# Performance work log

Measured on AMD Instinct MI355X. Metric: run time of the kernel, lower is better.

Reference implementation:

```python
import jax, jax.numpy as jnp
import numpy as np

CONTEXT = 2048
D_MODEL = 1024
HEAD = 64


def setup_inputs() -> dict:
    key = jax.random.key(0)
    kx, kk, kq, kv = jax.random.split(key, 4)
    s = 1.0 / np.sqrt(D_MODEL)  # ~ torch Linear init scale
    return {
        "x": jax.random.normal(kx, (8, CONTEXT, D_MODEL), dtype=jnp.float32),
        "Wk": jax.random.uniform(kk, (D_MODEL, HEAD), dtype=jnp.float32, minval=-s, maxval=s),
        "Wq": jax.random.uniform(kq, (D_MODEL, HEAD), dtype=jnp.float32, minval=-s, maxval=s),
        "Wv": jax.random.uniform(kv, (D_MODEL, HEAD), dtype=jnp.float32, minval=-s, maxval=s),
    }


def reference(x, Wk, Wq, Wv):
    b, t, c = x.shape
    k = jnp.einsum("btc,ch->bth", x, Wk)
    q = jnp.einsum("btc,ch->bth", x, Wq)
    v = jnp.einsum("btc,ch->bth", x, Wv)
    # NOTE: original scales by c**-0.5 (embedding dim), not head_size**-0.5
    scores = jnp.einsum("bqh,bkh->bqk", q, k) * (c ** -0.5)
    causal = jnp.tril(jnp.ones((t, t), dtype=bool))
    scores = jnp.where(causal, scores, jnp.float32(-jnp.inf))
    weights = jax.nn.softmax(scores, axis=-1)
    return jnp.einsum("bqk,bkh->bqh", weights, v)
```

## Files before the change

kernel.cpp:

```cpp
#include <hip/hip_runtime.h>
#include <hip/hip_bf16.h>

#define CTX 2048
#define DM  1024
#define HD  64
#define BATCH 8
#define NSLOT 144

typedef __attribute__((ext_vector_type(8))) short bf16x8;
typedef __attribute__((ext_vector_type(4))) float f32x4;

__device__ inline unsigned short f2bf(float f) {
    unsigned int u = __float_as_uint(f);
    unsigned int r = (u + 0x7fffu + ((u >> 16) & 1u)) >> 16;
    return (unsigned short)r;
}

__device__ inline bf16x8 pack8(const float4& f0, const float4& f1) {
    union { bf16x8 v; __hip_bfloat162 h[4]; } u;
    u.h[0] = __float22bfloat162_rn(make_float2(f0.x, f0.y));
    u.h[1] = __float22bfloat162_rn(make_float2(f0.z, f0.w));
    u.h[2] = __float22bfloat162_rn(make_float2(f1.x, f1.y));
    u.h[3] = __float22bfloat162_rn(make_float2(f1.z, f1.w));
    return u.v;
}

__device__ __forceinline__ int chunk_prefix(int qi) {
    int q4 = qi >> 2, r = qi & 3;
    return qi + 2 * q4 * (q4 - 1) + q4 * r;
}

__global__ __launch_bounds__(256) void wtrans(
    const float* __restrict__ Wq, const float* __restrict__ Wk,
    const float* __restrict__ Wv, unsigned short* __restrict__ wt)
{
    __shared__ __align__(16) unsigned short tile[64][72];
    const int m  = blockIdx.y;
    const int k0 = blockIdx.x * 64;
    const float* W = (m == 0) ? Wq : (m == 1) ? Wk : Wv;
    const int tid = threadIdx.x;
    const int c   = tid & 63, kk = tid >> 6;
    #pragma unroll
    for (int i = 0; i < 16; i++) {
        int kl = kk + i * 4;
        tile[c][kl] = f2bf(W[(size_t)(k0 + kl) * HD + c]);
    }
    __syncthreads();
    const int c2 = tid >> 2, seg = tid & 3;
    bf16x8 a = *reinterpret_cast<const bf16x8*>(&tile[c2][seg * 16]);
    bf16x8 b = *reinterpret_cast<const bf16x8*>(&tile[c2][seg * 16 + 8]);
    unsigned short* dst = wt + (size_t)(m * 64 + c2) * DM + k0 + seg * 16;
    *reinterpret_cast<bf16x8*>(dst)     = a;
    *reinterpret_cast<bf16x8*>(dst + 8) = b;
}

__global__ __launch_bounds__(512) void qkv_gemm(
    const float* __restrict__ x, const unsigned short* __restrict__ wt,
    unsigned short* __restrict__ q, unsigned short* __restrict__ k,
    unsigned short* __restrict__ vt)
{
    __shared__ __align__(16) unsigned short wsT[2][192 * 64];
    __shared__ __align__(16) unsigned short xsB[2][32 * 64];

    const int tid  = threadIdx.x, lane = tid & 63, w = tid >> 6;
    const int wr   = w >> 2, wc = w & 3;
    const int m0   = (int)blockIdx.x * 32;
    const int lcol = lane & 15, g = lane >> 4;

    const int wc_c   = tid >> 3;
    const int wc_par = tid & 7;
    const int xrow   = tid >> 3;
    const int xpar   = tid & 7;

    f32x4 acc[3];
    #pragma unroll
    for (int cf = 0; cf < 3; cf++) acc[cf] = (f32x4)0.f;

    bf16x8 rwA[3], rwB[3];
    float4 rxA0, rxA1, rxB0, rxB1;

    auto ldA = [&](int k0) {
        #pragma unroll
        for (int i = 0; i < 3; i++)
            rwA[i] = *reinterpret_cast<const bf16x8*>(wt + (size_t)(wc_c + i * 64) * DM + k0 + wc_par * 8);
        if (tid < 256) {
            const float* src = x + (size_t)(m0 + xrow) * DM + k0 + xpar * 8;
            rxA0 = *reinterpret_cast<const float4*>(src);
            rxA1 = *reinterpret_cast<const float4*>(src + 4);
        }
    };
    auto ldB = [&](int k0) {
        #pragma unroll
        for (int i = 0; i < 3; i++)
            rwB[i] = *reinterpret_cast<const bf16x8*>(wt + (size_t)(wc_c + i * 64) * DM + k0 + wc_par * 8);
        if (tid < 256) {
            const float* src = x + (size_t)(m0 + xrow) * DM + k0 + xpar * 8;
            rxB0 = *reinterpret_cast<const float4*>(src);
            rxB1 = *reinterpret_cast<const float4*>(src + 4);
        }
    };
    auto stA = [&](int buf) {
        char* wb = reinterpret_cast<char*>(wsT[buf]);
        char* xb = reinterpret_cast<char*>(xsB[buf]);
        #pragma unroll
        for (int i = 0; i < 3; i++) {
            int c = wc_c + i * 64;
            *reinterpret_cast<bf16x8*>(wb + ((c * 128 + wc_par * 16) ^ ((c & 7) << 4))) = rwA[i];
        }
        if (tid < 256)
            *reinterpret_cast<bf16x8*>(xb + ((xrow * 128 + xpar * 16) ^ ((xrow & 7) << 4))) = pack8(rxA0, rxA1);
    };
    auto stB = [&](int buf) {
        char* wb = reinterpret_cast<char*>(wsT[buf]);
        char* xb = reinterpret_cast<char*>(xsB[buf]);
        #pragma unroll
        for (int i = 0; i < 3; i++) {
            int c = wc_c + i * 64;
            *reinterpret_cast<bf16x8*>(wb + ((c * 128 + wc_par * 16) ^ ((c & 7) << 4))) = rwB[i];
        }
        if (tid < 256)
            *reinterpret_cast<bf16x8*>(xb + ((xrow * 128 + xpar * 16) ^ ((xrow & 7) << 4))) = pack8(rxB0, rxB1);
    };
    auto compute = [&](int buf) {
        char* wb = reinterpret_cast<char*>(wsT[buf]);
        char* xb = reinterpret_cast<char*>(xsB[buf]);
        #pragma unroll
        for (int kc = 0; kc < 2; kc++) {
            const int arow = wr * 16 + lcol;
            bf16x8 a = *reinterpret_cast<const bf16x8*>(
                xb + ((arow * 128 + kc * 64 + g * 16) ^ ((arow & 7) << 4)));
            #pragma unroll
            for (int cf = 0; cf < 3; cf++) {
                const int c = wc * 48 + cf * 16 + lcol;
                bf16x8 b = *reinterpret_cast<const bf16x8*>(
                    wb + ((c * 128 + kc * 64 + g * 16) ^ ((c & 7) << 4)));
                acc[cf] = __builtin_amdgcn_mfma_f32_16x16x32_bf16(a, b, acc[cf], 0, 0, 0);
            }
        }
    };

    ldA(0); ldB(64);
    stA(0);
    __syncthreads();

    #pragma unroll 1
    for (int t = 0; t < 16; t += 2) {
        if (t + 2 < 16) ldA((t + 2) * 64);
        compute(0);
        stB(1);
        __syncthreads();
        if (t + 3 < 16) ldB((t + 3) * 64);
        compute(1);
        if (t + 2 < 16) stA(0);
        __syncthreads();
    }

    const float QSCALE = 0.03125f * 1.4426950408889634f;
    #pragma unroll
    for (int cf = 0; cf < 3; cf++)
        #pragma unroll
        for (int r = 0; r < 4; r++) {
            int row = m0 + wr * 16 + g * 4 + r;
            int col = wc * 48 + cf * 16 + lcol;
            int bb = row >> 11, tt = row & (CTX - 1);
            if (col < 64)       q[(size_t)row * HD + col] = f2bf(acc[cf][r] * QSCALE);
            else if (col < 128) k[(size_t)row * HD + (col - 64)] = f2bf(acc[cf][r]);
            else                vt[(size_t)bb * HD * CTX + (size_t)(col - 128) * CTX + tt] = f2bf(acc[cf][r]);
        }
}

__global__ __launch_bounds__(256) void attn_fa(
    const unsigned short* __restrict__ qg, const unsigned short* __restrict__ kg,
    const unsigned short* __restrict__ vtg, unsigned short* __restrict__ po,
    float* __restrict__ ml)
{
    __shared__ __align__(16) unsigned short ks[64 * 64];
    __shared__ __align__(16) unsigned short vs[64 * 64];
    __shared__ __align__(16) float pf[4][16][68];

    const int tid  = threadIdx.x, lane = tid & 63, w = tid >> 6;
    const int bid  = blockIdx.x;
    const int b    = blockIdx.y;
    int qi = 31;
    while (chunk_prefix(qi) > bid) qi--;
    const int c  = bid - chunk_prefix(qi);
    const int t0 = c * 4, t1 = min(t0 + 3, qi);
    const int rb = qi * 64 + w * 16;
    const int lcol = lane & 15, g = lane >> 4, lrow = g << 2;
    const size_t base  = (size_t)b * CTX * HD;
    const size_t vbase = (size_t)b * HD * CTX;
    char* ksb = reinterpret_cast<char*>(ks);
    char* vsb = reinterpret_cast<char*>(vs);

    bf16x8 qa[2];
    #pragma unroll
    for (int kc = 0; kc < 2; kc++)
        qa[kc] = *reinterpret_cast<const bf16x8*>(
            qg + base + (size_t)(rb + lcol) * HD + kc * 32 + 8 * g);

    f32x4 o[4];
    #pragma unroll
    for (int dc = 0; dc < 4; dc++) o[dc] = (f32x4)0.f;
    float lsum[4] = {0.f, 0.f, 0.f, 0.f};

    const int r0 = tid >> 3, p0 = tid & 7, r1 = 32 + r0;
    bf16x8 kreg0, kreg1, vreg0, vreg1;

    auto ld = [&](int t) {
        const int j0 = t * 64;
        kreg0 = *reinterpret_cast<const bf16x8*>(kg + base + (size_t)(j0 + r0) * HD + p0 * 8);
        kreg1 = *reinterpret_cast<const bf16x8*>(kg + base + (size_t)(j0 + r1) * HD + p0 * 8);
        vreg0 = *reinterpret_cast<const bf16x8*>(vtg + vbase + (size_t)r0 * CTX + j0 + p0 * 8);
        vreg1 = *reinterpret_cast<const bf16x8*>(vtg + vbase + (size_t)r1 * CTX + j0 + p0 * 8);
    };
    auto st = [&]() {
        *reinterpret_cast<bf16x8*>(ksb + ((r0 * 128 + p0 * 16) ^ ((r0 & 7) << 4))) = kreg0;
        *reinterpret_cast<bf16x8*>(ksb + ((r1 * 128 + p0 * 16) ^ ((r1 & 7) << 4))) = kreg1;
        *reinterpret_cast<bf16x8*>(vsb + ((r0 * 128 + p0 * 16) ^ ((r0 & 7) << 4))) = vreg0;
        *reinterpret_cast<bf16x8*>(vsb + ((r1 * 128 + p0 * 16) ^ ((r1 & 7) << 4))) = vreg1;
    };

    ld(t0);
    for (int t = t0; t <= t1; t++) {
        __syncthreads();
        st();
        __syncthreads();
        if (t < t1) ld(t + 1);
        const int j0 = t * 64;

        f32x4 s[4];
        #pragma unroll
        for (int ch = 0; ch < 4; ch++) {
            s[ch] = (f32x4)0.f;
            #pragma unroll
            for (int kc = 0; kc < 2; kc++) {
                const int krow = ch * 16 + lcol;
                bf16x8 kf = *reinterpret_cast<const bf16x8*>(
                    ksb + ((krow * 128 + kc * 64 + g * 16) ^ ((krow & 7) << 4)));
                s[ch] = __builtin_amdgcn_mfma_f32_16x16x32_bf16(qa[kc], kf, s[ch], 0, 0, 0);
            }
        }

        if (t == qi) {
            #pragma unroll
            for (int ch = 0; ch < 4; ch++)
                #pragma unroll
                for (int r = 0; r < 4; r++)
                    if (j0 + ch * 16 + lcol > rb + lrow + r) s[ch][r] = -1e30f;
        }

        #pragma unroll
        for (int ch = 0; ch < 4; ch++)
            #pragma unroll
            for (int r = 0; r < 4; r++) {
                float p = exp2f(s[ch][r]);
                lsum[r] += p;
                pf[w][lrow + r][ch * 16 + lcol] = p;
            }

        bf16x8 pa[2];
        #pragma unroll
        for (int kc = 0; kc < 2; kc++) {
            const float* prow = &pf[w][lcol][0];
            float4 f0 = *reinterpret_cast<const float4*>(prow + kc * 32 + 8 * g);
            float4 f1 = *reinterpret_cast<const float4*>(prow + kc * 32 + 8 * g + 4);
            pa[kc] = pack8(f0, f1);
        }

        #pragma unroll
        for (int dc = 0; dc < 4; dc++)
            #pragma unroll
            for (int kc = 0; kc < 2; kc++) {
                const int vrow = dc * 16 + lcol;
                bf16x8 vf = *reinterpret_cast<const bf16x8*>(
                    vsb + ((vrow * 128 + kc * 64 + g * 16) ^ ((vrow & 7) << 4)));
                o[dc] = __builtin_amdgcn_mfma_f32_16x16x32_bf16(pa[kc], vf, o[dc], 0, 0, 0);
            }
    }

    const size_t sl = (size_t)b * NSLOT + bid;
    #pragma unroll
    for (int dc = 0; dc < 4; dc++)
        #pragma unroll
        for (int r = 0; r < 4; r++)
            po[sl * 4096 + (size_t)(w * 16 + lrow + r) * 64 + dc * 16 + lcol] = f2bf(o[dc][r]);
    #pragma unroll
    for (int r = 0; r < 4; r++) {
        float x = lsum[r];
        x += __shfl_xor(x, 1);
        x += __shfl_xor(x, 2);
        x += __shfl_xor(x, 4);
        x += __shfl_xor(x, 8);
        lsum[r] = x;
    }
    if (lcol == 0) {
        #pragma unroll
        for (int r = 0; r < 4; r++)
            ml[sl * 64 + w * 16 + lrow + r] = lsum[r];
    }
}

__global__ __launch_bounds__(256) void attn_merge(
    const unsigned short* __restrict__ po, const float* __restrict__ ml,
    float* __restrict__ out)
{
    const int qi = blockIdx.x, b = blockIdx.y;
    const int nch = (qi >> 2) + 1;
    const int s0  = chunk_prefix(qi);
    const int f8  = threadIdx.x & 7;
    const int r0  = threadIdx.x >> 3;
    const size_t obase = (size_t)b * CTX * HD;

    #pragma unroll
    for (int half = 0; half < 2; half++) {
        const int row = half * 32 + r0;
        float L = 0.f;
        float acc[8];
        #pragma unroll
        for (int j = 0; j < 8; j++) acc[j] = 0.f;
        for (int cc = 0; cc < nch; cc++) {
            size_t sl = (size_t)b * NSLOT + s0 + cc;
            L += ml[sl * 64 + row];
            bf16x8 v8 = *reinterpret_cast<const bf16x8*>(po + sl * 4096 + (size_t)row * 64 + f8 * 8);
            #pragma unroll
            for (int j = 0; j < 8; j++)
                acc[j] += __uint_as_float(((unsigned)(unsigned short)v8[j]) << 16);
        }
        const float inv = 1.f / L;
        float4 o0 = make_float4(acc[0] * inv, acc[1] * inv, acc[2] * inv, acc[3] * inv);
        float4 o1 = make_float4(acc[4] * inv, acc[5] * inv, acc[6] * inv, acc[7] * inv);
        float* dst = out + obase + (size_t)(qi * 64 + row) * HD + f8 * 8;
        *reinterpret_cast<float4*>(dst)     = o0;
        *reinterpret_cast<float4*>(dst + 4) = o1;
    }
}

extern "C" void kernel_launch(void* const* d_in, const int* in_sizes, int n_in,
                              void* d_out, int out_size, void* d_ws, size_t ws_size,
                              hipStream_t stream) {
    const float* x  = (const float*)d_in[0];
    const float* Wk = (const float*)d_in[1];
    const float* Wq = (const float*)d_in[2];
    const float* Wv = (const float*)d_in[3];
    float* outp = (float*)d_out;

    const size_t n = (size_t)BATCH * CTX * HD;
    unsigned short* qb  = (unsigned short*)d_ws;
    unsigned short* kb  = qb + n;
    unsigned short* vtb = kb + n;
    unsigned short* wtb = vtb + n;
    unsigned short* pob = wtb + 192 * 1024;
    float*          mlb = (float*)(pob + (size_t)BATCH * NSLOT * 4096);

    wtrans<<<dim3(16, 3), dim3(256), 0, stream>>>(Wq, Wk, Wv, wtb);
    qkv_gemm<<<dim3(16384 / 32), dim3(512), 0, stream>>>(x, wtb, qb, kb, vtb);
    attn_fa<<<dim3(NSLOT, BATCH), dim3(256), 0, stream>>>(qb, kb, vtb, pob, mlb);
    attn_merge<<<dim3(32, BATCH), dim3(256), 0, stream>>>(pob, mlb, outp);
}
```

Baseline: 53.90 us.

## Read QKV weights directly from global, swizzle P buffer, vectorize partial-output stores

```diff
diff --git a/kernel.cpp b/kernel.cpp
--- a/kernel.cpp
+++ b/kernel.cpp
@@ -23,6 +23,15 @@
     u.h[2] = __float22bfloat162_rn(make_float2(f1.x, f1.y));
     u.h[3] = __float22bfloat162_rn(make_float2(f1.z, f1.w));
     return u.v;
+}
+
+__device__ inline uint2 pack4(const float4& f) {
+    __hip_bfloat162 h0 = __float22bfloat162_rn(make_float2(f.x, f.y));
+    __hip_bfloat162 h1 = __float22bfloat162_rn(make_float2(f.z, f.w));
+    uint2 r;
+    __builtin_memcpy(&r.x, &h0, 4);
+    __builtin_memcpy(&r.y, &h1, 4);
+    return r;
 }
 
 __device__ __forceinline__ int chunk_prefix(int qi) {
@@ -59,99 +68,58 @@
     unsigned short* __restrict__ q, unsigned short* __restrict__ k,
     unsigned short* __restrict__ vt)
 {
-    __shared__ __align__(16) unsigned short wsT[2][192 * 64];
-    __shared__ __align__(16) unsigned short xsB[2][32 * 64];
+    __shared__ __align__(16) unsigned short xs[2][32 * 64];
 
     const int tid  = threadIdx.x, lane = tid & 63, w = tid >> 6;
     const int wr   = w >> 2, wc = w & 3;
     const int m0   = (int)blockIdx.x * 32;
     const int lcol = lane & 15, g = lane >> 4;
 
-    const int wc_c   = tid >> 3;
-    const int wc_par = tid & 7;
-    const int xrow   = tid >> 3;
-    const int xpar   = tid & 7;
+    const int xrow = tid >> 4, xseg = tid & 15;
+    const float* xsrc = x + (size_t)(m0 + xrow) * DM + xseg * 4;
+    const int xoff = (xrow * 128 + xseg * 8) ^ ((xrow & 7) << 4);
+
+    const unsigned short* wbase = wt + (size_t)(wc * 48 + lcol) * DM + g * 8;
 
     f32x4 acc[3];
     #pragma unroll
     for (int cf = 0; cf < 3; cf++) acc[cf] = (f32x4)0.f;
 
-    bf16x8 rwA[3], rwB[3];
-    float4 rxA0, rxA1, rxB0, rxB1;
-
-    auto ldA = [&](int k0) {
-        #pragma unroll
-        for (int i = 0; i < 3; i++)
-            rwA[i] = *reinterpret_cast<const bf16x8*>(wt + (size_t)(wc_c + i * 64) * DM + k0 + wc_par * 8);
-        if (tid < 256) {
-            const float* src = x + (size_t)(m0 + xrow) * DM + k0 + xpar * 8;
-            rxA0 = *reinterpret_cast<const float4*>(src);
-            rxA1 = *reinterpret_cast<const float4*>(src + 4);
-        }
+    float4 ra, rb;
+    auto ld = [&](int k0) { return *reinterpret_cast<const float4*>(xsrc + k0); };
+    auto st = [&](const float4& v, int buf) {
+        *reinterpret_cast<uint2*>(reinterpret_cast<char*>(xs[buf]) + xoff) = pack4(v);
     };
-    auto ldB = [&](int k0) {
-        #pragma unroll
-        for (int i = 0; i < 3; i++)
-            rwB[i] = *reinterpret_cast<const bf16x8*>(wt + (size_t)(wc_c + i * 64) * DM + k0 + wc_par * 8);
-        if (tid < 256) {
-            const float* src = x + (size_t)(m0 + xrow) * DM + k0 + xpar * 8;
-            rxB0 = *reinterpret_cast<const float4*>(src);
-            rxB1 = *reinterpret_cast<const float4*>(src + 4);
-        }
-    };
-    auto stA = [&](int buf) {
-        char* wb = reinterpret_cast<char*>(wsT[buf]);
-        char* xb = reinterpret_cast<char*>(xsB[buf]);
-        #pragma unroll
-        for (int i = 0; i < 3; i++) {
-            int c = wc_c + i * 64;
-            *reinterpret_cast<bf16x8*>(wb + ((c * 128 + wc_par * 16) ^ ((c & 7) << 4))) = rwA[i];
-        }
-        if (tid < 256)
-            *reinterpret_cast<bf16x8*>(xb + ((xrow * 128 + xpar * 16) ^ ((xrow & 7) << 4))) = pack8(rxA0, rxA1);
-    };
-    auto stB = [&](int buf) {
-        char* wb = reinterpret_cast<char*>(wsT[buf]);
-        char* xb = reinterpret_cast<char*>(xsB[buf]);
-        #pragma unroll
-        for (int i = 0; i < 3; i++) {
-            int c = wc_c + i * 64;
-            *reinterpret_cast<bf16x8*>(wb + ((c * 128 + wc_par * 16) ^ ((c & 7) << 4))) = rwB[i];
-        }
-        if (tid < 256)
-            *reinterpret_cast<bf16x8*>(xb + ((xrow * 128 + xpar * 16) ^ ((xrow & 7) << 4))) = pack8(rxB0, rxB1);
-    };
-    auto compute = [&](int buf) {
-        char* wb = reinterpret_cast<char*>(wsT[buf]);
-        char* xb = reinterpret_cast<char*>(xsB[buf]);
+    auto compute = [&](int buf, int k0) {
+        char* xb = reinterpret_cast<char*>(xs[buf]);
+        const int arow = wr * 16 + lcol;
         #pragma unroll
         for (int kc = 0; kc < 2; kc++) {
-            const int arow = wr * 16 + lcol;
             bf16x8 a = *reinterpret_cast<const bf16x8*>(
                 xb + ((arow * 128 + kc * 64 + g * 16) ^ ((arow & 7) << 4)));
             #pragma unroll
             for (int cf = 0; cf < 3; cf++) {
-                const int c = wc * 48 + cf * 16 + lcol;
                 bf16x8 b = *reinterpret_cast<const bf16x8*>(
-                    wb + ((c * 128 + kc * 64 + g * 16) ^ ((c & 7) << 4)));
+                    wbase + (size_t)cf * 16 * DM + k0 + kc * 32);
                 acc[cf] = __builtin_amdgcn_mfma_f32_16x16x32_bf16(a, b, acc[cf], 0, 0, 0);
             }
         }
     };
 
-    ldA(0); ldB(64);
-    stA(0);
+    ra = ld(0);
+    rb = ld(64);
+    st(ra, 0);
     __syncthreads();
 
     #pragma unroll 1
     for (int t = 0; t < 16; t += 2) {
-        if (t + 2 < 16) ldA((t + 2) * 64);
-        compute(0);
-        stB(1);
+        if (t + 2 < 16) ra = ld((t + 2) * 64);
+        compute(0, t * 64);
+        st(rb, 1);
         __syncthreads();
-        if (t + 3 < 16) ldB((t + 3) * 64);
-        compute(1);
-        if (t + 2 < 16) stA(0);
+        if (t + 3 < 16) rb = ld((t + 3) * 64);
+        compute(1, (t + 1) * 64);
+        if (t + 2 < 16) st(ra, 0);
         __syncthreads();
     }
 
@@ -176,7 +144,7 @@
 {
     __shared__ __align__(16) unsigned short ks[64 * 64];
     __shared__ __align__(16) unsigned short vs[64 * 64];
-    __shared__ __align__(16) float pf[4][16][68];
+    __shared__ __align__(16) float pf[4][16 * 64];
 
     const int tid  = threadIdx.x, lane = tid & 63, w = tid >> 6;
     const int bid  = blockIdx.x;
@@ -191,6 +159,7 @@
     const size_t vbase = (size_t)b * HD * CTX;
     char* ksb = reinterpret_cast<char*>(ks);
     char* vsb = reinterpret_cast<char*>(vs);
+    char* pb  = reinterpret_cast<char*>(pf[w]);
 
     bf16x8 qa[2];
     #pragma unroll
@@ -255,15 +224,19 @@
             for (int r = 0; r < 4; r++) {
                 float p = exp2f(s[ch][r]);
                 lsum[r] += p;
-                pf[w][lrow + r][ch * 16 + lcol] = p;
+                const int row = lrow + r;
+                *reinterpret_cast<float*>(
+                    pb + ((row * 256 + (ch * 16 + lcol) * 4) ^ ((row & 7) << 4))) = p;
             }
 
         bf16x8 pa[2];
+        const int rswz = (lcol & 7) << 4;
         #pragma unroll
         for (int kc = 0; kc < 2; kc++) {
-            const float* prow = &pf[w][lcol][0];
-            float4 f0 = *reinterpret_cast<const float4*>(prow + kc * 32 + 8 * g);
-            float4 f1 = *reinterpret_cast<const float4*>(prow + kc * 32 + 8 * g + 4);
+            float4 f0 = *reinterpret_cast<const float4*>(
+                pb + ((lcol * 256 + kc * 128 + g * 32) ^ rswz));
+            float4 f1 = *reinterpret_cast<const float4*>(
+                pb + ((lcol * 256 + kc * 128 + g * 32 + 16) ^ rswz));
             pa[kc] = pack8(f0, f1);
         }
 
@@ -282,8 +255,22 @@
     #pragma unroll
     for (int dc = 0; dc < 4; dc++)
         #pragma unroll
-        for (int r = 0; r < 4; r++)
-            po[sl * 4096 + (size_t)(w * 16 + lrow + r) * 64 + dc * 16 + lcol] = f2bf(o[dc][r]);
+        for (int r = 0; r < 4; r++) {
+            const int row = lrow + r;
+            *reinterpret_cast<float*>(
+                pb + ((row * 256 + (dc * 16 + lcol) * 4) ^ ((row & 7) << 4))) = o[dc][r];
+        }
+    {
+        const int orow = lcol;
+        const int rswz = (orow & 7) << 4;
+        float4 a0 = *reinterpret_cast<const float4*>(pb + ((orow * 256 + g * 64)      ^ rswz));
+        float4 a1 = *reinterpret_cast<const float4*>(pb + ((orow * 256 + g * 64 + 16) ^ rswz));
+        float4 a2 = *reinterpret_cast<const float4*>(pb + ((orow * 256 + g * 64 + 32) ^ rswz));
+        float4 a3 = *reinterpret_cast<const float4*>(pb + ((orow * 256 + g * 64 + 48) ^ rswz));
+        unsigned short* dst = po + sl * 4096 + (size_t)(w * 16 + orow) * 64 + g * 16;
+        *reinterpret_cast<bf16x8*>(dst)     = pack8(a0, a1);
+        *reinterpret_cast<bf16x8*>(dst + 8) = pack8(a2, a3);
+    }
     #pragma unroll
     for (int r = 0; r < 4; r++) {
         float x = lsum[r];
```

Result: slower. 84.01 us (+55.9%).

## Double-buffer attention K/V tiles, store P as bf16, rechunk work and deepen GEMM prefetch

Applied to the files above, without the earlier changes.

```diff
diff --git a/kernel.cpp b/kernel.cpp
--- a/kernel.cpp
+++ b/kernel.cpp
@@ -5,7 +5,7 @@
 #define DM  1024
 #define HD  64
 #define BATCH 8
-#define NSLOT 144
+#define NSLOT 119
 
 typedef __attribute__((ext_vector_type(8))) short bf16x8;
 typedef __attribute__((ext_vector_type(4))) float f32x4;
@@ -25,9 +25,16 @@
     return u.v;
 }
 
+__device__ inline unsigned int packpair(float a, float b) {
+    __hip_bfloat162 h = __float22bfloat162_rn(make_float2(a, b));
+    unsigned int r;
+    __builtin_memcpy(&r, &h, 4);
+    return r;
+}
+
 __device__ __forceinline__ int chunk_prefix(int qi) {
-    int q4 = qi >> 2, r = qi & 3;
-    return qi + 2 * q4 * (q4 - 1) + q4 * r;
+    int mf = qi / 5, r = qi - mf * 5;
+    return 5 * mf * (mf + 1) / 2 + r * (mf + 1);
 }
 
 __global__ __launch_bounds__(256) void wtrans(
@@ -54,7 +61,7 @@
     *reinterpret_cast<bf16x8*>(dst + 8) = b;
 }
 
-__global__ __launch_bounds__(512) void qkv_gemm(
+__global__ __launch_bounds__(512, 4) void qkv_gemm(
     const float* __restrict__ x, const unsigned short* __restrict__ wt,
     unsigned short* __restrict__ q, unsigned short* __restrict__ k,
     unsigned short* __restrict__ vt)
@@ -76,50 +83,33 @@
     #pragma unroll
     for (int cf = 0; cf < 3; cf++) acc[cf] = (f32x4)0.f;
 
-    bf16x8 rwA[3], rwB[3];
-    float4 rxA0, rxA1, rxB0, rxB1;
-
-    auto ldA = [&](int k0) {
+    bf16x8 rw[2][3];
+    float4 rx[4][2];
+
+    auto ldW = [&](int k0, int s) {
         #pragma unroll
         for (int i = 0; i < 3; i++)
-            rwA[i] = *reinterpret_cast<const bf16x8*>(wt + (size_t)(wc_c + i * 64) * DM + k0 + wc_par * 8);
+            rw[s][i] = *reinterpret_cast<const bf16x8*>(
+                wt + (size_t)(wc_c + i * 64) * DM + k0 + wc_par * 8);
+    };
+    auto ldX = [&](int k0, int s) {
         if (tid < 256) {
             const float* src = x + (size_t)(m0 + xrow) * DM + k0 + xpar * 8;
-            rxA0 = *reinterpret_cast<const float4*>(src);
-            rxA1 = *reinterpret_cast<const float4*>(src + 4);
-        }
-    };
-    auto ldB = [&](int k0) {
-        #pragma unroll
-        for (int i = 0; i < 3; i++)
-            rwB[i] = *reinterpret_cast<const bf16x8*>(wt + (size_t)(wc_c + i * 64) * DM + k0 + wc_par * 8);
-        if (tid < 256) {
-            const float* src = x + (size_t)(m0 + xrow) * DM + k0 + xpar * 8;
-            rxB0 = *reinterpret_cast<const float4*>(src);
-            rxB1 = *reinterpret_cast<const float4*>(src + 4);
-        }
-    };
-    auto stA = [&](int buf) {
+            rx[s][0] = *reinterpret_cast<const float4*>(src);
+            rx[s][1] = *reinterpret_cast<const float4*>(src + 4);
+        }
+    };
+    auto st = [&](int sw, int sx, int buf) {
         char* wb = reinterpret_cast<char*>(wsT[buf]);
         char* xb = reinterpret_cast<char*>(xsB[buf]);
         #pragma unroll
         for (int i = 0; i < 3; i++) {
             int c = wc_c + i * 64;
-            *reinterpret_cast<bf16x8*>(wb + ((c * 128 + wc_par * 16) ^ ((c & 7) << 4))) = rwA[i];
+            *reinterpret_cast<bf16x8*>(wb + ((c * 128 + wc_par * 16) ^ ((c & 7) << 4))) = rw[sw][i];
         }
         if (tid < 256)
-            *reinterpret_cast<bf16x8*>(xb + ((xrow * 128 + xpar * 16) ^ ((xrow & 7) << 4))) = pack8(rxA0, rxA1);
-    };
-    auto stB = [&](int buf) {
-        char* wb = reinterpret_cast<char*>(wsT[buf]);
-        char* xb = reinterpret_cast<char*>(xsB[buf]);
-        #pragma unroll
-        for (int i = 0; i < 3; i++) {
-            int c = wc_c + i * 64;
-            *reinterpret_cast<bf16x8*>(wb + ((c * 128 + wc_par * 16) ^ ((c & 7) << 4))) = rwB[i];
-        }
-        if (tid < 256)
-            *reinterpret_cast<bf16x8*>(xb + ((xrow * 128 + xpar * 16) ^ ((xrow & 7) << 4))) = pack8(rxB0, rxB1);
+            *reinterpret_cast<bf16x8*>(xb + ((xrow * 128 + xpar * 16) ^ ((xrow & 7) << 4))) =
+                pack8(rx[sx][0], rx[sx][1]);
     };
     auto compute = [&](int buf) {
         char* wb = reinterpret_cast<char*>(wsT[buf]);
@@ -139,19 +129,17 @@
         }
     };
 
-    ldA(0); ldB(64);
-    stA(0);
+    ldW(0, 0); ldW(64, 1);
+    ldX(0, 0); ldX(64, 1); ldX(128, 2); ldX(192, 3);
+    st(0, 0, 0);
     __syncthreads();
 
-    #pragma unroll 1
-    for (int t = 0; t < 16; t += 2) {
-        if (t + 2 < 16) ldA((t + 2) * 64);
-        compute(0);
-        stB(1);
-        __syncthreads();
-        if (t + 3 < 16) ldB((t + 3) * 64);
-        compute(1);
-        if (t + 2 < 16) stA(0);
+    #pragma unroll
+    for (int t = 0; t < 16; t++) {
+        if (t + 2 < 16) ldW((t + 2) * 64, t & 1);
+        if (t + 4 < 16) ldX((t + 4) * 64, t & 3);
+        compute(t & 1);
+        if (t + 1 < 16) st((t + 1) & 1, (t + 1) & 3, (t + 1) & 1);
         __syncthreads();
     }
 
@@ -174,9 +162,9 @@
     const unsigned short* __restrict__ vtg, unsigned short* __restrict__ po,
     float* __restrict__ ml)
 {
-    __shared__ __align__(16) unsigned short ks[64 * 64];
-    __shared__ __align__(16) unsigned short vs[64 * 64];
-    __shared__ __align__(16) float pf[4][16][68];
+    __shared__ __align__(16) unsigned short ks[2][64 * 64];
+    __shared__ __align__(16) unsigned short vs[2][64 * 64];
+    __shared__ __align__(16) unsigned short pfb[4][16 * 64];
 
     const int tid  = threadIdx.x, lane = tid & 63, w = tid >> 6;
     const int bid  = blockIdx.x;
@@ -184,13 +172,12 @@
     int qi = 31;
     while (chunk_prefix(qi) > bid) qi--;
     const int c  = bid - chunk_prefix(qi);
-    const int t0 = c * 4, t1 = min(t0 + 3, qi);
+    const int t0 = c * 5, t1 = min(t0 + 4, qi);
     const int rb = qi * 64 + w * 16;
     const int lcol = lane & 15, g = lane >> 4, lrow = g << 2;
     const size_t base  = (size_t)b * CTX * HD;
     const size_t vbase = (size_t)b * HD * CTX;
-    char* ksb = reinterpret_cast<char*>(ks);
-    char* vsb = reinterpret_cast<char*>(vs);
+    char* pb = reinterpret_cast<char*>(pfb[w]);
 
     bf16x8 qa[2];
     #pragma unroll
@@ -213,7 +200,9 @@
         vreg0 = *reinterpret_cast<const bf16x8*>(vtg + vbase + (size_t)r0 * CTX + j0 + p0 * 8);
         vreg1 = *reinterpret_cast<const bf16x8*>(vtg + vbase + (size_t)r1 * CTX + j0 + p0 * 8);
     };
-    auto st = [&]() {
+    auto st = [&](int buf) {
+        char* ksb = reinterpret_cast<char*>(ks[buf]);
+        char* vsb = reinterpret_cast<char*>(vs[buf]);
         *reinterpret_cast<bf16x8*>(ksb + ((r0 * 128 + p0 * 16) ^ ((r0 & 7) << 4))) = kreg0;
         *reinterpret_cast<bf16x8*>(ksb + ((r1 * 128 + p0 * 16) ^ ((r1 & 7) << 4))) = kreg1;
         *reinterpret_cast<bf16x8*>(vsb + ((r0 * 128 + p0 * 16) ^ ((r0 & 7) << 4))) = vreg0;
@@ -221,11 +210,14 @@
     };
 
     ld(t0);
+    st(0);
+    if (t0 < t1) ld(t0 + 1);
+
     for (int t = t0; t <= t1; t++) {
+        const int p = (t - t0) & 1;
         __syncthreads();
-        st();
-        __syncthreads();
-        if (t < t1) ld(t + 1);
+        char* ksb = reinterpret_cast<char*>(ks[p]);
+        char* vsb = reinterpret_cast<char*>(vs[p]);
         const int j0 = t * 64;
 
         f32x4 s[4];
@@ -253,19 +245,22 @@
         for (int ch = 0; ch < 4; ch++)
             #pragma unroll
             for (int r = 0; r < 4; r++) {
-                float p = exp2f(s[ch][r]);
-                lsum[r] += p;
-                pf[w][lrow + r][ch * 16 + lcol] = p;
+                float pv = exp2f(s[ch][r]);
+                lsum[r] += pv;
+                float pr = __shfl_xor(pv, 1);
+                if (!(lane & 1)) {
+                    const int row = lrow + r;
+                    *reinterpret_cast<unsigned int*>(
+                        pb + ((row * 128 + (ch * 16 + lcol) * 2) ^ ((row & 7) << 4))) =
+                        packpair(pv, pr);
+                }
             }
 
         bf16x8 pa[2];
         #pragma unroll
-        for (int kc = 0; kc < 2; kc++) {
-            const float* prow = &pf[w][lcol][0];
-            float4 f0 = *reinterpret_cast<const float4*>(prow + kc * 32 + 8 * g);
-            float4 f1 = *reinterpret_cast<const float4*>(prow + kc * 32 + 8 * g + 4);
-            pa[kc] = pack8(f0, f1);
-        }
+        for (int kc = 0; kc < 2; kc++)
+            pa[kc] = *reinterpret_cast<const bf16x8*>(
+                pb + ((lcol * 128 + kc * 64 + g * 16) ^ ((lcol & 7) << 4)));
 
         #pragma unroll
         for (int dc = 0; dc < 4; dc++)
@@ -276,22 +271,41 @@
                     vsb + ((vrow * 128 + kc * 64 + g * 16) ^ ((vrow & 7) << 4)));
                 o[dc] = __builtin_amdgcn_mfma_f32_16x16x32_bf16(pa[kc], vf, o[dc], 0, 0, 0);
             }
+
+        if (t < t1) st(p ^ 1);
+        if (t + 2 <= t1) ld(t + 2);
     }
 
     const size_t sl = (size_t)b * NSLOT + bid;
     #pragma unroll
     for (int dc = 0; dc < 4; dc++)
         #pragma unroll
-        for (int r = 0; r < 4; r++)
-            po[sl * 4096 + (size_t)(w * 16 + lrow + r) * 64 + dc * 16 + lcol] = f2bf(o[dc][r]);
+        for (int r = 0; r < 4; r++) {
+            float pr = __shfl_xor(o[dc][r], 1);
+            if (!(lane & 1)) {
+                const int row = lrow + r;
+                *reinterpret_cast<unsigned int*>(
+                    pb + ((row * 128 + (dc * 16 + lcol) * 2) ^ ((row & 7) << 4))) =
+                    packpair(o[dc][r], pr);
+            }
+        }
+    {
+        const int orow = lcol;
+        const int rswz = (orow & 7) << 4;
+        bf16x8 o0 = *reinterpret_cast<const bf16x8*>(pb + ((orow * 128 + g * 32) ^ rswz));
+        bf16x8 o1 = *reinterpret_cast<const bf16x8*>(pb + ((orow * 128 + g * 32 + 16) ^ rswz));
+        unsigned short* dst = po + sl * 4096 + (size_t)(w * 16 + orow) * 64 + g * 16;
+        *reinterpret_cast<bf16x8*>(dst)     = o0;
+        *reinterpret_cast<bf16x8*>(dst + 8) = o1;
+    }
     #pragma unroll
     for (int r = 0; r < 4; r++) {
-        float x = lsum[r];
-        x += __shfl_xor(x, 1);
-        x += __shfl_xor(x, 2);
-        x += __shfl_xor(x, 4);
-        x += __shfl_xor(x, 8);
-        lsum[r] = x;
+        float xv = lsum[r];
+        xv += __shfl_xor(xv, 1);
+        xv += __shfl_xor(xv, 2);
+        xv += __shfl_xor(xv, 4);
+        xv += __shfl_xor(xv, 8);
+        lsum[r] = xv;
     }
     if (lcol == 0) {
         #pragma unroll
@@ -305,7 +319,7 @@
     float* __restrict__ out)
 {
     const int qi = blockIdx.x, b = blockIdx.y;
-    const int nch = (qi >> 2) + 1;
+    const int nch = (qi + 5) / 5;
     const int s0  = chunk_prefix(qi);
     const int f8  = threadIdx.x & 7;
     const int r0  = threadIdx.x >> 3;
```

Result: slower. 62.81 us (+16.5%).
